# Kernel tuning notes

Hardware: AMD Instinct MI355X
Metric: run time of the kernel (lower is better)

The kernel has to match this reference:

```python
import jax, jax.numpy as jnp
import numpy as np

N = 8192          # mesh vertices
E = 49152         # directed edges (avg degree 6)
M = 25            # kernel_size per pseudo-dim
DIM = 3           # pseudo-coordinate dim
K = M ** DIM      # 15625 weight matrices per layer
S = 2 ** DIM      # 8 nonzero degree-1 B-spline products per edge
LC, UC = -0.22703196, 0.36853024   # curvature range
LM, UM = 1.2585511, 1.648841       # myelin range
R = 10.0
LAYER_DIMS = [(2, 32), (32, 64), (64, 64), (64, 32), (32, 1)]


def transform(x):
    # rescale curv/myelin channels into [-R, R] with clamping (matches torch masking)
    t0 = (x[:, 0] - LC) / (UC - LC) * (2.0 * R) - R
    t1 = (x[:, 1] - LM) / (UM - LM) * (2.0 * R) - R
    return jnp.stack([jnp.clip(t0, -R, R), jnp.clip(t1, -R, R)], axis=1)


def spline_basis(pseudo):
    # open B-spline, degree 1: v in [0, M-1); 8 corner products per edge
    v = pseudo * (M - 1)
    lo = jnp.floor(v)
    f = v - lo                                                    # [E, DIM]
    lo = lo.astype(jnp.int32)
    bits = (jnp.arange(S)[:, None] >> jnp.arange(DIM)[None, :]) & 1   # [S, DIM]
    oh = bits.astype(pseudo.dtype)
    basis = jnp.prod(oh[None] * f[:, None, :] + (1.0 - oh[None]) * (1.0 - f[:, None, :]), axis=-1)  # [E, S]
    strides = (M ** jnp.arange(DIM)).astype(jnp.int32)
    wi = jnp.sum((lo[:, None, :] + bits[None]) * strides[None, None, :], axis=-1)  # [E, S] kernel indices
    return basis, wi


def spline_conv(h, src, dst, basis, wi, W, root, bias):
    xj = h[src]                                             # [E, Fin] gather
    msg = jnp.zeros((xj.shape[0], W.shape[2]), h.dtype)
    for s in range(S):                                      # fixed 8-way basis loop
        msg = msg + basis[:, s, None] * jnp.einsum('ei,eio->eo', xj, W[wi[:, s]])
    agg = jax.ops.segment_sum(msg, dst, num_segments=N)     # scatter-sum (norm=False)
    return agg + h @ root + bias


def setup_inputs() -> dict:
    key = jax.random.key(0)
    ks = jax.random.split(key, 3 + 2 * len(LAYER_DIMS))
    inp = {
        "x": jax.random.normal(ks[0], (N, 2), dtype=jnp.float32),
        "edge_index": jax.random.randint(ks[1], (2, E), 0, N),
        "pseudo": jax.random.uniform(ks[2], (E, DIM), dtype=jnp.float32),
    }
    for i, (fi, fo) in enumerate(LAYER_DIMS):
        kw, kr = ks[3 + 2 * i], ks[4 + 2 * i]
        inp[f"W{i+1}"] = jax.random.normal(kw, (K, fi, fo), dtype=jnp.float32) / np.float32(np.sqrt(fi * S))
        inp[f"root{i+1}"] = jax.random.normal(kr, (fi, fo), dtype=jnp.float32) / np.float32(np.sqrt(fi))
        inp[f"b{i+1}"] = jnp.zeros((fo,), dtype=jnp.float32)
    return inp


def reference(x, edge_index, pseudo, W1, root1, b1, W2, root2, b2, W3, root3, b3,
              W4, root4, b4, W5, root5, b5):
    src, dst = edge_index[0], edge_index[1]
    basis, wi = spline_basis(pseudo)   # shared across all 5 layers, as in the torch model
    h = transform(x)
    for W, r, b in ((W1, root1, b1), (W2, root2, b2), (W3, root3, b3),
                    (W4, root4, b4), (W5, root5, b5)):
        h = jax.nn.elu(spline_conv(h, src, dst, basis, wi, W, r, b))
    return h.reshape(-1)
```

## Files before the change

### kernel.cpp

```cpp
#include <hip/hip_runtime.h>
#include <math.h>

#define NV 8192
#define EV 49152
#define KK 15625

typedef __attribute__((ext_vector_type(8))) short bf16x8;
typedef __attribute__((ext_vector_type(4))) float f32x4;

__device__ __forceinline__ void atomAddF(float* p, float v) {
    unsafeAtomicAdd(p, v);
}

__device__ __forceinline__ unsigned short bf16rne(float x) {
    unsigned u = __float_as_uint(x);
    unsigned r = u + 0x7FFFu + ((u >> 16) & 1u);
    return (unsigned short)(r >> 16);
}
__device__ __forceinline__ float bf16tof(unsigned short h) {
    return __uint_as_float(((unsigned)h) << 16);
}

__device__ __forceinline__ void edge_frac(const float* __restrict__ pseudo, int e,
                                          float f[3], int lo[3]) {
#pragma unroll
    for (int j = 0; j < 3; ++j) {
        float v = pseudo[e * 3 + j] * 24.0f;
        float fl = floorf(v);
        int l = (int)fl;
        l = l < 0 ? 0 : (l > 23 ? 23 : l);
        lo[j] = l;
        f[j] = v - (float)l;
    }
}

__global__ void prep_kernel(const float* __restrict__ x, float* __restrict__ h0,
                            int* __restrict__ counts, float* __restrict__ agg) {
    int gt = blockIdx.x * blockDim.x + threadIdx.x;
    if (gt < NV) {
        const float LC = -0.22703196f, UC = 0.36853024f;
        const float LM = 1.2585511f, UM = 1.648841f;
        const float R = 10.0f;
        float t0 = (x[gt * 2 + 0] - LC) / (UC - LC) * (2.0f * R) - R;
        float t1 = (x[gt * 2 + 1] - LM) / (UM - LM) * (2.0f * R) - R;
        h0[gt * 2 + 0] = fminf(fmaxf(t0, -R), R);
        h0[gt * 2 + 1] = fminf(fmaxf(t1, -R), R);
    }
    if (gt < KK) counts[gt] = 0;
    if (gt < NV * 64) agg[gt] = 0.0f;
}

__global__ void hist_kernel(const float* __restrict__ pseudo, int* __restrict__ counts) {
    int e = blockIdx.x * blockDim.x + threadIdx.x;
    if (e >= EV) return;
    float f[3]; int lo[3];
    edge_frac(pseudo, e, f, lo);
#pragma unroll
    for (int s = 0; s < 8; ++s) {
        int wi = (lo[0] + (s & 1)) + 25 * (lo[1] + ((s >> 1) & 1)) + 625 * (lo[2] + ((s >> 2) & 1));
        atomicAdd(&counts[wi], 1);
    }
}

__global__ void scan_kernel(const int* __restrict__ counts, int* __restrict__ offsets,
                            int* __restrict__ cursor) {
    __shared__ int sums[256];
    const int CH = 62;
    int t = threadIdx.x;
    int base = t * CH;
    int s = 0;
    for (int i = 0; i < CH; ++i) {
        int idx = base + i;
        if (idx < KK) s += counts[idx];
    }
    sums[t] = s;
    __syncthreads();
    for (int d = 1; d < 256; d <<= 1) {
        int v = (t >= d) ? sums[t - d] : 0;
        __syncthreads();
        sums[t] += v;
        __syncthreads();
    }
    int run = (t > 0) ? sums[t - 1] : 0;
    for (int i = 0; i < CH; ++i) {
        int idx = base + i;
        if (idx < KK) {
            offsets[idx] = run;
            cursor[idx] = run;
            run += counts[idx];
        }
    }
    if (t == 255) offsets[KK] = run;
}

__global__ void scatter_kernel(const float* __restrict__ pseudo, const int* __restrict__ ei,
                               int* __restrict__ cursor,
                               int* __restrict__ pair_src, int2* __restrict__ pair_db) {
    int e = blockIdx.x * blockDim.x + threadIdx.x;
    if (e >= EV) return;
    float f[3]; int lo[3];
    edge_frac(pseudo, e, f, lo);
    int src = ei[e];
    int dst = ei[EV + e];
#pragma unroll
    for (int s = 0; s < 8; ++s) {
        float b = ((s & 1) ? f[0] : 1.0f - f[0]) *
                  (((s >> 1) & 1) ? f[1] : 1.0f - f[1]) *
                  (((s >> 2) & 1) ? f[2] : 1.0f - f[2]);
        int wi = (lo[0] + (s & 1)) + 25 * (lo[1] + ((s >> 1) & 1)) + 625 * (lo[2] + ((s >> 2) & 1));
        int pos = atomicAdd(&cursor[wi], 1);
        pair_src[pos] = src;
        pair_db[pos] = make_int2(dst, __float_as_int(b));
    }
}

template <int FIN, int FOUT>
__global__ __launch_bounds__(256) void conv_v8(
    const unsigned short* __restrict__ hhi, const unsigned short* __restrict__ hlo,
    const float* __restrict__ W,
    const int* __restrict__ offsets, const int* __restrict__ pair_src,
    const int2* __restrict__ pair_db, float* __restrict__ agg) {
    constexpr int KT = FIN / 32;
    constexpr int NT = FOUT / 16;
    const int J = KK * NT;
    int w = threadIdx.x >> 6;
    int lane = threadIdx.x & 63;
    int l15 = lane & 15;
    int lg = lane >> 4;
    int nwaves = gridDim.x * 4;

    for (int job = blockIdx.x * 4 + w; job < J; job += nwaves) {
        int k = job / NT;
        int nslice = job - k * NT;
        int start = offsets[k];
        int n = offsets[k + 1] - start;
        if (n <= 0) continue;

        const float* Wk = W + (size_t)k * (FIN * FOUT) + nslice * 16 + l15;
        bf16x8 Bh[KT], Bl[KT];
#pragma unroll
        for (int k0 = 0; k0 < KT; ++k0)
#pragma unroll
            for (int i = 0; i < 8; ++i) {
                float wv = Wk[(size_t)(k0 * 32 + lg * 8 + i) * FOUT];
                unsigned short hi = bf16rne(wv);
                unsigned short lo = bf16rne(wv - bf16tof(hi));
                Bh[k0][i] = (short)hi;
                Bl[k0][i] = (short)lo;
            }

        const int* psrc = pair_src + start;
        const int2* pdb = pair_db + start;

        for (int m0 = 0; m0 < n; m0 += 16) {
            int ra = m0 + l15;
            int src = psrc[ra < n ? ra : 0];
            const unsigned short* rhi = hhi + (size_t)src * FIN + lg * 8;
            const unsigned short* rlo = hlo + (size_t)src * FIN + lg * 8;

            f32x4 acc = (f32x4){0.f, 0.f, 0.f, 0.f};
#pragma unroll
            for (int k0 = 0; k0 < KT; ++k0) {
                bf16x8 Ah = *(const bf16x8*)(rhi + k0 * 32);
                bf16x8 Al = *(const bf16x8*)(rlo + k0 * 32);
                acc = __builtin_amdgcn_mfma_f32_16x16x32_bf16(Ah, Bh[k0], acc, 0, 0, 0);
                acc = __builtin_amdgcn_mfma_f32_16x16x32_bf16(Ah, Bl[k0], acc, 0, 0, 0);
                acc = __builtin_amdgcn_mfma_f32_16x16x32_bf16(Al, Bh[k0], acc, 0, 0, 0);
            }

#pragma unroll
            for (int j = 0; j < 4; ++j) {
                int rm = m0 + lg * 4 + j;
                if (rm < n) {
                    int2 db = pdb[rm];
                    atomAddF(&agg[(size_t)db.x * FOUT + nslice * 16 + l15],
                             acc[j] * __int_as_float(db.y));
                }
            }
        }
    }
}

__global__ __launch_bounds__(256) void conv_l1(
    const float* __restrict__ h, const float* __restrict__ W,
    const int* __restrict__ offsets, const int* __restrict__ pair_src,
    const int2* __restrict__ pair_db, float* __restrict__ agg) {
    int w = threadIdx.x >> 6;
    int lane = threadIdx.x & 63;
    int o = lane & 31;
    int g = lane >> 5;
    int nwaves = gridDim.x * 4;
    const float2* h2 = (const float2*)h;
    for (int k = blockIdx.x * 4 + w; k < KK; k += nwaves) {
        int start = offsets[k];
        int n = offsets[k + 1] - start;
        if (n <= 0) continue;
        const float* Wk = W + (size_t)k * 64;
        float w0 = Wk[o], w1 = Wk[32 + o];
        for (int r = g; r < n; r += 2) {
            int src = pair_src[start + r];
            int2 db = pair_db[start + r];
            float b = __int_as_float(db.y);
            float2 xv = h2[src];
            atomAddF(&agg[(size_t)db.x * 32 + o], b * (xv.x * w0 + xv.y * w1));
        }
    }
}

__global__ __launch_bounds__(256) void conv_f1(
    const unsigned short* __restrict__ hhi, const unsigned short* __restrict__ hlo,
    const float* __restrict__ W,
    const int* __restrict__ offsets, const int* __restrict__ pair_src,
    const int2* __restrict__ pair_db, float* __restrict__ agg) {
    int w = threadIdx.x >> 6;
    int lane = threadIdx.x & 63;
    int i = lane & 31;
    int g = lane >> 5;
    int nwaves = gridDim.x * 4;
    for (int k = blockIdx.x * 4 + w; k < KK; k += nwaves) {
        int start = offsets[k];
        int n = offsets[k + 1] - start;
        if (n <= 0) continue;
        float wk = W[(size_t)k * 32 + i];
        for (int r = g; r < n; r += 2) {
            int src = pair_src[start + r];
            int2 db = pair_db[start + r];
            float b = __int_as_float(db.y);
            float hv = bf16tof(hhi[(size_t)src * 32 + i]) + bf16tof(hlo[(size_t)src * 32 + i]);
            float val = hv * wk * b;
#pragma unroll
            for (int d = 16; d >= 1; d >>= 1) val += __shfl_xor(val, d, 32);
            if (i == 0) atomAddF(&agg[db.x], val);
        }
    }
}

__global__ void node1_kernel(const float* __restrict__ h, float* __restrict__ agg,
                             const float* __restrict__ root, const float* __restrict__ bias,
                             unsigned short* __restrict__ ohi, unsigned short* __restrict__ olo) {
    int idx = blockIdx.x * blockDim.x + threadIdx.x;
    if (idx >= NV * 64) return;
    if (idx < NV * 32) {
        int n = idx >> 5, o = idx & 31;
        float acc = agg[idx] + bias[o] + h[n * 2] * root[o] + h[n * 2 + 1] * root[32 + o];
        float v = acc > 0.0f ? acc : expm1f(acc);
        unsigned short hi = bf16rne(v);
        ohi[idx] = hi;
        olo[idx] = bf16rne(v - bf16tof(hi));
    }
    agg[idx] = 0.0f;
}

template <int FIN, int FOUT>
__global__ void node_p(const unsigned short* __restrict__ hhi,
                       const unsigned short* __restrict__ hlo, float* __restrict__ agg,
                       const float* __restrict__ root, const float* __restrict__ bias,
                       unsigned short* __restrict__ ohi, unsigned short* __restrict__ olo) {
    int idx = blockIdx.x * blockDim.x + threadIdx.x;
    if (idx >= NV * 64) return;
    if (idx < NV * FOUT) {
        int n = idx / FOUT, o = idx % FOUT;
        float acc = agg[idx] + bias[o];
#pragma unroll
        for (int i = 0; i < FIN; ++i) {
            float hv = bf16tof(hhi[(size_t)n * FIN + i]) + bf16tof(hlo[(size_t)n * FIN + i]);
            acc += hv * root[i * FOUT + o];
        }
        float v = acc > 0.0f ? acc : expm1f(acc);
        unsigned short hi = bf16rne(v);
        ohi[idx] = hi;
        olo[idx] = bf16rne(v - bf16tof(hi));
    }
    agg[idx] = 0.0f;
}

__global__ void node5_kernel(const unsigned short* __restrict__ hhi,
                             const unsigned short* __restrict__ hlo,
                             const float* __restrict__ agg, const float* __restrict__ root,
                             const float* __restrict__ bias, float* __restrict__ out) {
    int n = blockIdx.x * blockDim.x + threadIdx.x;
    if (n >= NV) return;
    float acc = agg[n] + bias[0];
#pragma unroll
    for (int i = 0; i < 32; ++i) {
        float hv = bf16tof(hhi[(size_t)n * 32 + i]) + bf16tof(hlo[(size_t)n * 32 + i]);
        acc += hv * root[i];
    }
    out[n] = acc > 0.0f ? acc : expm1f(acc);
}

extern "C" void kernel_launch(void* const* d_in, const int* in_sizes, int n_in,
                              void* d_out, int out_size, void* d_ws, size_t ws_size,
                              hipStream_t stream) {
    const float* x      = (const float*)d_in[0];
    const int*   ei     = (const int*)d_in[1];
    const float* pseudo = (const float*)d_in[2];
    const float* W1 = (const float*)d_in[3];
    const float* r1 = (const float*)d_in[4];
    const float* b1 = (const float*)d_in[5];
    const float* W2 = (const float*)d_in[6];
    const float* r2 = (const float*)d_in[7];
    const float* b2 = (const float*)d_in[8];
    const float* W3 = (const float*)d_in[9];
    const float* r3 = (const float*)d_in[10];
    const float* b3 = (const float*)d_in[11];
    const float* W4 = (const float*)d_in[12];
    const float* r4 = (const float*)d_in[13];
    const float* b4 = (const float*)d_in[14];
    const float* W5 = (const float*)d_in[15];
    const float* r5 = (const float*)d_in[16];
    const float* b5 = (const float*)d_in[17];

    char* ws = (char*)d_ws;
    size_t off = 0;
    auto alloc = [&](size_t bytes) {
        void* p = ws + off;
        off += (bytes + 255) & ~(size_t)255;
        return p;
    };
    int*   counts   = (int*)alloc(KK * sizeof(int));
    int*   offsets  = (int*)alloc((KK + 1) * sizeof(int));
    int*   cursor   = (int*)alloc(KK * sizeof(int));
    int*   pair_src = (int*)alloc((size_t)EV * 8 * sizeof(int));
    int2*  pair_db  = (int2*)alloc((size_t)EV * 8 * sizeof(int2));
    float* h0       = (float*)alloc((size_t)NV * 2 * sizeof(float));
    unsigned short* pAhi = (unsigned short*)alloc((size_t)NV * 64 * sizeof(unsigned short));
    unsigned short* pAlo = (unsigned short*)alloc((size_t)NV * 64 * sizeof(unsigned short));
    unsigned short* pBhi = (unsigned short*)alloc((size_t)NV * 64 * sizeof(unsigned short));
    unsigned short* pBlo = (unsigned short*)alloc((size_t)NV * 64 * sizeof(unsigned short));
    float* agg      = (float*)alloc((size_t)NV * 64 * sizeof(float));

    const int NGRID = (NV * 64 + 255) / 256;
    const int CGRID = 2048;

    prep_kernel<<<NGRID, 256, 0, stream>>>(x, h0, counts, agg);
    hist_kernel<<<(EV + 255) / 256, 256, 0, stream>>>(pseudo, counts);
    scan_kernel<<<1, 256, 0, stream>>>(counts, offsets, cursor);
    scatter_kernel<<<(EV + 255) / 256, 256, 0, stream>>>(pseudo, ei, cursor, pair_src, pair_db);

    conv_l1<<<CGRID, 256, 0, stream>>>(h0, W1, offsets, pair_src, pair_db, agg);
    node1_kernel<<<NGRID, 256, 0, stream>>>(h0, agg, r1, b1, pAhi, pAlo);

    conv_v8<32, 64><<<CGRID, 256, 0, stream>>>(pAhi, pAlo, W2, offsets, pair_src, pair_db, agg);
    node_p<32, 64><<<NGRID, 256, 0, stream>>>(pAhi, pAlo, agg, r2, b2, pBhi, pBlo);

    conv_v8<64, 64><<<CGRID, 256, 0, stream>>>(pBhi, pBlo, W3, offsets, pair_src, pair_db, agg);
    node_p<64, 64><<<NGRID, 256, 0, stream>>>(pBhi, pBlo, agg, r3, b3, pAhi, pAlo);

    conv_v8<64, 32><<<CGRID, 256, 0, stream>>>(pAhi, pAlo, W4, offsets, pair_src, pair_db, agg);
    node_p<64, 32><<<NGRID, 256, 0, stream>>>(pAhi, pAlo, agg, r4, b4, pBhi, pBlo);

    conv_f1<<<CGRID, 256, 0, stream>>>(pBhi, pBlo, W5, offsets, pair_src, pair_db, agg);
    node5_kernel<<<(NV + 255) / 256, 256, 0, stream>>>(pBhi, pBlo, agg, r5, b5, (float*)d_out);
}
```

Before: 551.1 us.

## Assign contiguous job ranges per wave and prefetch next weights and source indices

New measurement: 594.2 us. 7.8% more time.

```diff
diff --git a/kernel.cpp b/kernel.cpp
--- a/kernel.cpp
+++ b/kernel.cpp
@@ -115,7 +115,7 @@
 }
 
 template <int FIN, int FOUT>
-__global__ __launch_bounds__(256) void conv_v8(
+__global__ __launch_bounds__(256) void conv_v9(
     const unsigned short* __restrict__ hhi, const unsigned short* __restrict__ hlo,
     const float* __restrict__ W,
     const int* __restrict__ offsets, const int* __restrict__ pair_src,
@@ -128,36 +128,55 @@
     int l15 = lane & 15;
     int lg = lane >> 4;
     int nwaves = gridDim.x * 4;
-
-    for (int job = blockIdx.x * 4 + w; job < J; job += nwaves) {
+    int gwave = blockIdx.x * 4 + w;
+    int bpw = (J + nwaves - 1) / nwaves;
+    int j0 = gwave * bpw;
+    int j1 = j0 + bpw < J ? j0 + bpw : J;
+    if (j0 >= j1) return;
+
+    float vW[KT * 8];
+    auto ldW = [&](int job) {
         int k = job / NT;
-        int nslice = job - k * NT;
+        int ns = job - k * NT;
+        const float* Wk = W + (size_t)k * (FIN * FOUT) + ns * 16 + l15;
+#pragma unroll
+        for (int k0 = 0; k0 < KT; ++k0)
+#pragma unroll
+            for (int i = 0; i < 8; ++i)
+                vW[k0 * 8 + i] = Wk[(size_t)(k0 * 32 + lg * 8 + i) * FOUT];
+    };
+
+    ldW(j0);
+    for (int j = j0; j < j1; ++j) {
+        bf16x8 Bh[KT], Bl[KT];
+#pragma unroll
+        for (int k0 = 0; k0 < KT; ++k0)
+#pragma unroll
+            for (int i = 0; i < 8; ++i) {
+                float wv = vW[k0 * 8 + i];
+                unsigned short hi = bf16rne(wv);
+                Bh[k0][i] = (short)hi;
+                Bl[k0][i] = (short)bf16rne(wv - bf16tof(hi));
+            }
+        if (j + 1 < j1) ldW(j + 1);
+
+        int k = j / NT;
+        int nslice = j - k * NT;
         int start = offsets[k];
         int n = offsets[k + 1] - start;
         if (n <= 0) continue;
-
-        const float* Wk = W + (size_t)k * (FIN * FOUT) + nslice * 16 + l15;
-        bf16x8 Bh[KT], Bl[KT];
-#pragma unroll
-        for (int k0 = 0; k0 < KT; ++k0)
-#pragma unroll
-            for (int i = 0; i < 8; ++i) {
-                float wv = Wk[(size_t)(k0 * 32 + lg * 8 + i) * FOUT];
-                unsigned short hi = bf16rne(wv);
-                unsigned short lo = bf16rne(wv - bf16tof(hi));
-                Bh[k0][i] = (short)hi;
-                Bl[k0][i] = (short)lo;
-            }
-
         const int* psrc = pair_src + start;
         const int2* pdb = pair_db + start;
 
+        int src = psrc[l15 < n ? l15 : 0];
         for (int m0 = 0; m0 < n; m0 += 16) {
-            int ra = m0 + l15;
-            int src = psrc[ra < n ? ra : 0];
             const unsigned short* rhi = hhi + (size_t)src * FIN + lg * 8;
             const unsigned short* rlo = hlo + (size_t)src * FIN + lg * 8;
-
+            int srcn = 0;
+            if (m0 + 16 < n) {
+                int ra = m0 + 16 + l15;
+                srcn = psrc[ra < n ? ra : 0];
+            }
             f32x4 acc = (f32x4){0.f, 0.f, 0.f, 0.f};
 #pragma unroll
             for (int k0 = 0; k0 < KT; ++k0) {
@@ -167,16 +186,16 @@
                 acc = __builtin_amdgcn_mfma_f32_16x16x32_bf16(Ah, Bl[k0], acc, 0, 0, 0);
                 acc = __builtin_amdgcn_mfma_f32_16x16x32_bf16(Al, Bh[k0], acc, 0, 0, 0);
             }
-
-#pragma unroll
-            for (int j = 0; j < 4; ++j) {
-                int rm = m0 + lg * 4 + j;
+#pragma unroll
+            for (int jj = 0; jj < 4; ++jj) {
+                int rm = m0 + lg * 4 + jj;
                 if (rm < n) {
                     int2 db = pdb[rm];
                     atomAddF(&agg[(size_t)db.x * FOUT + nslice * 16 + l15],
-                             acc[j] * __int_as_float(db.y));
+                             acc[jj] * __int_as_float(db.y));
                 }
             }
+            src = srcn;
         }
     }
 }
@@ -190,8 +209,12 @@
     int o = lane & 31;
     int g = lane >> 5;
     int nwaves = gridDim.x * 4;
+    int gwave = blockIdx.x * 4 + w;
+    int bpw = (KK + nwaves - 1) / nwaves;
+    int k0 = gwave * bpw;
+    int k1 = k0 + bpw < KK ? k0 + bpw : KK;
     const float2* h2 = (const float2*)h;
-    for (int k = blockIdx.x * 4 + w; k < KK; k += nwaves) {
+    for (int k = k0; k < k1; ++k) {
         int start = offsets[k];
         int n = offsets[k + 1] - start;
         if (n <= 0) continue;
@@ -217,7 +240,11 @@
     int i = lane & 31;
     int g = lane >> 5;
     int nwaves = gridDim.x * 4;
-    for (int k = blockIdx.x * 4 + w; k < KK; k += nwaves) {
+    int gwave = blockIdx.x * 4 + w;
+    int bpw = (KK + nwaves - 1) / nwaves;
+    int kk0 = gwave * bpw;
+    int kk1 = kk0 + bpw < KK ? kk0 + bpw : KK;
+    for (int k = kk0; k < kk1; ++k) {
         int start = offsets[k];
         int n = offsets[k + 1] - start;
         if (n <= 0) continue;
@@ -341,13 +368,13 @@
     conv_l1<<<CGRID, 256, 0, stream>>>(h0, W1, offsets, pair_src, pair_db, agg);
     node1_kernel<<<NGRID, 256, 0, stream>>>(h0, agg, r1, b1, pAhi, pAlo);
 
-    conv_v8<32, 64><<<CGRID, 256, 0, stream>>>(pAhi, pAlo, W2, offsets, pair_src, pair_db, agg);
+    conv_v9<32, 64><<<CGRID, 256, 0, stream>>>(pAhi, pAlo, W2, offsets, pair_src, pair_db, agg);
     node_p<32, 64><<<NGRID, 256, 0, stream>>>(pAhi, pAlo, agg, r2, b2, pBhi, pBlo);
 
-    conv_v8<64, 64><<<CGRID, 256, 0, stream>>>(pBhi, pBlo, W3, offsets, pair_src, pair_db, agg);
+    conv_v9<64, 64><<<CGRID, 256, 0, stream>>>(pBhi, pBlo, W3, offsets, pair_src, pair_db, agg);
     node_p<64, 64><<<NGRID, 256, 0, stream>>>(pBhi, pBlo, agg, r3, b3, pAhi, pAlo);
 
-    conv_v8<64, 32><<<CGRID, 256, 0, stream>>>(pAhi, pAlo, W4, offsets, pair_src, pair_db, agg);
+    conv_v9<64, 32><<<CGRID, 256, 0, stream>>>(pAhi, pAlo, W4, offsets, pair_src, pair_db, agg);
     node_p<64, 32><<<NGRID, 256, 0, stream>>>(pAhi, pAlo, agg, r4, b4, pBhi, pBlo);
 
     conv_f1<<<CGRID, 256, 0, stream>>>(pBhi, pBlo, W5, offsets, pair_src, pair_db, agg);
```

## Stage weight matrices through LDS with coalesced float4 loads and register prefetch

Applied to the files above, without the earlier changes.

Result: no change. 561.6 us (+1.9%).

```diff
diff --git a/kernel.cpp b/kernel.cpp
--- a/kernel.cpp
+++ b/kernel.cpp
@@ -115,40 +115,71 @@
 }
 
 template <int FIN, int FOUT>
-__global__ __launch_bounds__(256) void conv_v8(
+__global__ __launch_bounds__(256) void conv_v10(
     const unsigned short* __restrict__ hhi, const unsigned short* __restrict__ hlo,
-    const float* __restrict__ W,
-    const int* __restrict__ offsets, const int* __restrict__ pair_src,
-    const int2* __restrict__ pair_db, float* __restrict__ agg) {
+    const float* __restrict__ W, const int* __restrict__ offsets,
+    const int* __restrict__ pair_src, const int2* __restrict__ pair_db,
+    float* __restrict__ agg) {
     constexpr int KT = FIN / 32;
     constexpr int NT = FOUT / 16;
-    const int J = KK * NT;
-    int w = threadIdx.x >> 6;
-    int lane = threadIdx.x & 63;
-    int l15 = lane & 15;
-    int lg = lane >> 4;
-    int nwaves = gridDim.x * 4;
-
-    for (int job = blockIdx.x * 4 + w; job < J; job += nwaves) {
-        int k = job / NT;
-        int nslice = job - k * NT;
-        int start = offsets[k];
-        int n = offsets[k + 1] - start;
+    constexpr int BPB = 4 / NT;
+    constexpr int WSZ = FIN * FOUT * BPB;
+    constexpr int NL4 = WSZ / 1024;
+    __shared__ float wlds[WSZ];
+    const float4* Wg4 = (const float4*)W;
+    const size_t TOT4 = (size_t)KK * FIN * FOUT / 4;
+    int t = threadIdx.x;
+    int w = t >> 6, lane = t & 63, l15 = lane & 15, lg = lane >> 4;
+    int widx = w / NT;
+    int ns = (w % NT) * 16;
+    int step = gridDim.x * BPB;
+    int iters = (KK + step - 1) / step;
+
+    float4 vst[NL4];
+    {
+        size_t b4 = (size_t)blockIdx.x * BPB * (FIN * FOUT / 4);
+#pragma unroll
+        for (int i = 0; i < NL4; ++i) {
+            size_t idx = b4 + (size_t)i * 256 + t;
+            vst[i] = idx < TOT4 ? Wg4[idx] : make_float4(0.f, 0.f, 0.f, 0.f);
+        }
+    }
+
+    for (int it = 0; it < iters; ++it) {
+        __syncthreads();
+#pragma unroll
+        for (int i = 0; i < NL4; ++i) ((float4*)wlds)[i * 256 + t] = vst[i];
+        __syncthreads();
+
+        int kbase = it * step + blockIdx.x * BPB;
+        int kb = kbase + widx;
+        bool has = kb < KK;
+        bf16x8 Bh[KT], Bl[KT];
+        if (has) {
+            const float* wl = wlds + widx * (FIN * FOUT) + ns + l15;
+#pragma unroll
+            for (int k0 = 0; k0 < KT; ++k0)
+#pragma unroll
+                for (int i = 0; i < 8; ++i) {
+                    float wv = wl[(size_t)(k0 * 32 + lg * 8 + i) * FOUT];
+                    unsigned short hi = bf16rne(wv);
+                    Bh[k0][i] = (short)hi;
+                    Bl[k0][i] = (short)bf16rne(wv - bf16tof(hi));
+                }
+        }
+        if (it + 1 < iters) {
+            size_t b4 = ((size_t)(it + 1) * step + (size_t)blockIdx.x * BPB) *
+                        (FIN * FOUT / 4);
+#pragma unroll
+            for (int i = 0; i < NL4; ++i) {
+                size_t idx = b4 + (size_t)i * 256 + t;
+                vst[i] = idx < TOT4 ? Wg4[idx] : make_float4(0.f, 0.f, 0.f, 0.f);
+            }
+        }
+        if (!has) continue;
+        int start = offsets[kb];
+        int n = offsets[kb + 1] - start;
         if (n <= 0) continue;
-
-        const float* Wk = W + (size_t)k * (FIN * FOUT) + nslice * 16 + l15;
-        bf16x8 Bh[KT], Bl[KT];
-#pragma unroll
-        for (int k0 = 0; k0 < KT; ++k0)
-#pragma unroll
-            for (int i = 0; i < 8; ++i) {
-                float wv = Wk[(size_t)(k0 * 32 + lg * 8 + i) * FOUT];
-                unsigned short hi = bf16rne(wv);
-                unsigned short lo = bf16rne(wv - bf16tof(hi));
-                Bh[k0][i] = (short)hi;
-                Bl[k0][i] = (short)lo;
-            }
-
         const int* psrc = pair_src + start;
         const int2* pdb = pair_db + start;
 
@@ -157,7 +188,6 @@
             int src = psrc[ra < n ? ra : 0];
             const unsigned short* rhi = hhi + (size_t)src * FIN + lg * 8;
             const unsigned short* rlo = hlo + (size_t)src * FIN + lg * 8;
-
             f32x4 acc = (f32x4){0.f, 0.f, 0.f, 0.f};
 #pragma unroll
             for (int k0 = 0; k0 < KT; ++k0) {
@@ -167,14 +197,13 @@
                 acc = __builtin_amdgcn_mfma_f32_16x16x32_bf16(Ah, Bl[k0], acc, 0, 0, 0);
                 acc = __builtin_amdgcn_mfma_f32_16x16x32_bf16(Al, Bh[k0], acc, 0, 0, 0);
             }
-
-#pragma unroll
-            for (int j = 0; j < 4; ++j) {
-                int rm = m0 + lg * 4 + j;
+#pragma unroll
+            for (int jj = 0; jj < 4; ++jj) {
+                int rm = m0 + lg * 4 + jj;
                 if (rm < n) {
                     int2 db = pdb[rm];
-                    atomAddF(&agg[(size_t)db.x * FOUT + nslice * 16 + l15],
-                             acc[j] * __int_as_float(db.y));
+                    atomAddF(&agg[(size_t)db.x * FOUT + ns + l15],
+                             acc[jj] * __int_as_float(db.y));
                 }
             }
         }
@@ -341,13 +370,13 @@
     conv_l1<<<CGRID, 256, 0, stream>>>(h0, W1, offsets, pair_src, pair_db, agg);
     node1_kernel<<<NGRID, 256, 0, stream>>>(h0, agg, r1, b1, pAhi, pAlo);
 
-    conv_v8<32, 64><<<CGRID, 256, 0, stream>>>(pAhi, pAlo, W2, offsets, pair_src, pair_db, agg);
+    conv_v10<32, 64><<<CGRID, 256, 0, stream>>>(pAhi, pAlo, W2, offsets, pair_src, pair_db, agg);
     node_p<32, 64><<<NGRID, 256, 0, stream>>>(pAhi, pAlo, agg, r2, b2, pBhi, pBlo);
 
-    conv_v8<64, 64><<<CGRID, 256, 0, stream>>>(pBhi, pBlo, W3, offsets, pair_src, pair_db, agg);
+    conv_v10<64, 64><<<CGRID, 256, 0, stream>>>(pBhi, pBlo, W3, offsets, pair_src, pair_db, agg);
     node_p<64, 64><<<NGRID, 256, 0, stream>>>(pBhi, pBlo, agg, r3, b3, pAhi, pAlo);
 
-    conv_v8<64, 32><<<CGRID, 256, 0, stream>>>(pAhi, pAlo, W4, offsets, pair_src, pair_db, agg);
+    conv_v10<64, 32><<<CGRID, 256, 0, stream>>>(pAhi, pAlo, W4, offsets, pair_src, pair_db, agg);
     node_p<64, 32><<<NGRID, 256, 0, stream>>>(pAhi, pAlo, agg, r4, b4, pBhi, pBlo);
 
     conv_f1<<<CGRID, 256, 0, stream>>>(pBhi, pBlo, W5, offsets, pair_src, pair_db, agg);
```
